# Performance work log

Hardware: AMD Instinct MI355X
Metric: run time of the kernel (lower is better)

## Reference

```python
import jax, jax.numpy as jnp
import numpy as np

P, D_IN, RANK, D_OUT, N = 64, 1024, 64, 1024, 4096


def setup_inputs() -> dict:
    key = jax.random.key(0)
    k1, k2, k3, k4, k5 = jax.random.split(key, 5)
    x = jax.random.normal(k1, (N, D_IN), dtype=jnp.float32)
    pids = jax.random.randint(k2, (N,), 0, P, dtype=jnp.int64)
    U = jax.random.normal(k3, (P, D_IN, RANK), dtype=jnp.float32) * 0.02
    V = jax.random.normal(k4, (P, RANK, D_OUT), dtype=jnp.float32) * 0.02
    bias = jax.random.normal(k5, (D_OUT,), dtype=jnp.float32)
    return {"x": x, "pids": pids, "U": U, "V": V, "bias": bias}


def reference(x, pids, U, V, bias):
    # Equivalent to: for each token n, out[n] = x[n] @ U[pids[n]] @ V[pids[n]] + bias
    # Computed as dense grouped GEMM over all partitions, then row-select by pid
    # (identical math to the masked per-partition loop in the torch module).
    h = jnp.einsum('nd,pdr->pnr', x, U)        # [P, N, R]
    o = jnp.einsum('pnr,pro->pno', h, V)       # [P, N, D_out]
    out = o[pids, jnp.arange(x.shape[0])] + bias  # select each token's own partition
    return out
```

## Files before the change

kernel.cpp:

```cpp
#include <hip/hip_runtime.h>
#include <hip/hip_bf16.h>

#define NP     64
#define D_IN   1024
#define RANK   64
#define D_OUT  1024
#define NTOK   4096
#define TM     64
#define BK     64
#define MT     128
#define KS     8
#define KW     (D_IN / KS)
#define OW     128
#define LDSTR  72

typedef __bf16 bf16x8 __attribute__((ext_vector_type(8)));
typedef float  f32x4  __attribute__((ext_vector_type(4)));

__device__ __forceinline__ unsigned short f2bf(float f) {
    unsigned u = __builtin_bit_cast(unsigned, f);
    u += 0x7FFFu + ((u >> 16) & 1u);
    return (unsigned short)(u >> 16);
}
__device__ __forceinline__ float bf2f(unsigned short s) {
    unsigned u = (unsigned)s << 16;
    return __builtin_bit_cast(float, u);
}
__device__ __forceinline__ bf16x8 pack8(float4 a, float4 b) {
    union { bf16x8 v; unsigned short s[8]; } r;
    r.s[0] = f2bf(a.x); r.s[1] = f2bf(a.y); r.s[2] = f2bf(a.z); r.s[3] = f2bf(a.w);
    r.s[4] = f2bf(b.x); r.s[5] = f2bf(b.y); r.s[6] = f2bf(b.z); r.s[7] = f2bf(b.w);
    return r.v;
}

__device__ __forceinline__ int swz_idx(int outer, int inner) {
    int blk = (inner >> 3) ^ ((outer >> 3) & 7);
    return outer * LDSTR + blk * 8 + (inner & 7);
}

__device__ __forceinline__ void decode_xcd(int b, int& tile, int& slice) {
    int g = b & 7;
    int l = b >> 3;
    slice = l >> 4;
    int m = l & 15;
    tile = (((m >> 1) << 3) | g) * 2 + (m & 1);
}

__global__ void bucket_kernel(const int* __restrict__ pids, int* __restrict__ meta) {
    __shared__ int counts[NP];
    __shared__ int cursor[NP];
    int tid = threadIdx.x;
    if (tid < NP) counts[tid] = 0;
    __syncthreads();
    for (int i = tid; i < NTOK / 4; i += 256) {
        int4 pv = reinterpret_cast<const int4*>(pids)[i];
        atomicAdd(&counts[pv.x & (NP - 1)], 1);
        atomicAdd(&counts[pv.y & (NP - 1)], 1);
        atomicAdd(&counts[pv.z & (NP - 1)], 1);
        atomicAdd(&counts[pv.w & (NP - 1)], 1);
    }
    __syncthreads();
    if (tid < 64) {
        int c = counts[tid];
        int ntp = (c + TM - 1) >> 6;
        int sc = c, st = ntp;
        for (int d = 1; d < 64; d <<= 1) {
            int vc = __shfl_up(sc, d);
            int vt = __shfl_up(st, d);
            if (tid >= d) { sc += vc; st += vt; }
        }
        int cbase = sc - c;
        int tb    = st - ntp;
        cursor[tid] = cbase;
        for (int t = 0; t < ntp; ++t) {
            int idx = tb + t;
            int rem = c - t * TM;
            int4 rec = {tid, cbase + t * TM, rem < TM ? rem : TM, 0};
            *reinterpret_cast<int4*>(meta + 16 + 4 * idx) = rec;
        }
        if (tid == 63) meta[0] = st;
    }
    __syncthreads();
    int* bucket = meta + 1024;
    for (int i = tid; i < NTOK / 4; i += 256) {
        int4 pv = reinterpret_cast<const int4*>(pids)[i];
        bucket[atomicAdd(&cursor[pv.x & (NP - 1)], 1)] = i * 4 + 0;
        bucket[atomicAdd(&cursor[pv.y & (NP - 1)], 1)] = i * 4 + 1;
        bucket[atomicAdd(&cursor[pv.z & (NP - 1)], 1)] = i * 4 + 2;
        bucket[atomicAdd(&cursor[pv.w & (NP - 1)], 1)] = i * 4 + 3;
    }
}

__global__ __launch_bounds__(256, 4) void h_kernel(
    const float* __restrict__ x, const float* __restrict__ U,
    const int* __restrict__ meta, unsigned short* __restrict__ Hpart)
{
    __shared__ __align__(16) unsigned short Us[2][RANK * LDSTR];
    __shared__ int toks[TM];

    int tile, ks;
    decode_xcd(blockIdx.x, tile, ks);
    int nt = meta[0];
    if (tile >= nt) return;
    int4 ti = *reinterpret_cast<const int4*>(meta + 16 + 4 * tile);
    int p = ti.x, off = ti.y, len = ti.z;

    int tid  = threadIdx.x;
    int lane = tid & 63;
    int w    = tid >> 6;
    int l15  = lane & 15;
    int l4   = lane >> 4;

    const int* bucket = meta + 1024;
    if (tid < TM) toks[tid] = (tid < len) ? bucket[off + tid] : -1;
    __syncthreads();

    int myrow = w * 16 + l15;
    int t = toks[myrow];
    bool valid = (t >= 0);
    const float* xrow = x + (size_t)(valid ? t : 0) * D_IN;
    const float* Up = U + (size_t)p * D_IN * RANK;

    int kbeg = ks * KW;
    int kk = tid >> 2;
    int q  = (tid & 3) * 16;

    float4 z{0,0,0,0};
    float4 c0a=z,c0b=z,c0c=z,c0d=z,c1a=z,c1b=z,c1c=z,c1d=z;
    if (valid) {
        const float* xp = xrow + kbeg + l4 * 8;
        c0a = *reinterpret_cast<const float4*>(xp);
        c0b = *reinterpret_cast<const float4*>(xp + 4);
        c0c = *reinterpret_cast<const float4*>(xp + 32);
        c0d = *reinterpret_cast<const float4*>(xp + 36);
        c1a = *reinterpret_cast<const float4*>(xp + 64);
        c1b = *reinterpret_cast<const float4*>(xp + 68);
        c1c = *reinterpret_cast<const float4*>(xp + 96);
        c1d = *reinterpret_cast<const float4*>(xp + 100);
    }

    f32x4 acc[4] = {};

    {
        const float* up = Up + (size_t)(kbeg + kk) * RANK + q;
#pragma unroll
        for (int i = 0; i < 4; ++i) {
            float4 v = *reinterpret_cast<const float4*>(up + i * 4);
            int r = q + i * 4;
            Us[0][swz_idx(r + 0, kk)] = f2bf(v.x);
            Us[0][swz_idx(r + 1, kk)] = f2bf(v.y);
            Us[0][swz_idx(r + 2, kk)] = f2bf(v.z);
            Us[0][swz_idx(r + 3, kk)] = f2bf(v.w);
        }
    }
    __syncthreads();

    float4 u10, u11, u12, u13;
    {
        const float* up = Up + (size_t)(kbeg + BK + kk) * RANK + q;
        u10 = *reinterpret_cast<const float4*>(up);
        u11 = *reinterpret_cast<const float4*>(up + 4);
        u12 = *reinterpret_cast<const float4*>(up + 8);
        u13 = *reinterpret_cast<const float4*>(up + 12);
    }

    {
        bf16x8 a0 = pack8(c0a, c0b);
        bf16x8 a1 = pack8(c0c, c0d);
#pragma unroll
        for (int k2 = 0; k2 < 2; ++k2) {
            int kof = k2 * 32 + l4 * 8;
            bf16x8 a = k2 ? a1 : a0;
#pragma unroll
            for (int ni = 0; ni < 4; ++ni) {
                bf16x8 b = *reinterpret_cast<const bf16x8*>(&Us[0][swz_idx(ni * 16 + l15, kof)]);
                acc[ni] = __builtin_amdgcn_mfma_f32_16x16x32_bf16(a, b, acc[ni], 0, 0, 0);
            }
        }
    }

    {
        float4 vv[4] = {u10, u11, u12, u13};
#pragma unroll
        for (int i = 0; i < 4; ++i) {
            int r = q + i * 4;
            Us[1][swz_idx(r + 0, kk)] = f2bf(vv[i].x);
            Us[1][swz_idx(r + 1, kk)] = f2bf(vv[i].y);
            Us[1][swz_idx(r + 2, kk)] = f2bf(vv[i].z);
            Us[1][swz_idx(r + 3, kk)] = f2bf(vv[i].w);
        }
    }
    __syncthreads();

    {
        bf16x8 a0 = pack8(c1a, c1b);
        bf16x8 a1 = pack8(c1c, c1d);
#pragma unroll
        for (int k2 = 0; k2 < 2; ++k2) {
            int kof = k2 * 32 + l4 * 8;
            bf16x8 a = k2 ? a1 : a0;
#pragma unroll
            for (int ni = 0; ni < 4; ++ni) {
                bf16x8 b = *reinterpret_cast<const bf16x8*>(&Us[1][swz_idx(ni * 16 + l15, kof)]);
                acc[ni] = __builtin_amdgcn_mfma_f32_16x16x32_bf16(a, b, acc[ni], 0, 0, 0);
            }
        }
    }

    unsigned short* hp = Hpart + ((size_t)ks * MT + tile) * (TM * RANK);
#pragma unroll
    for (int ni = 0; ni < 4; ++ni)
#pragma unroll
        for (int j = 0; j < 4; ++j) {
            int row = w * 16 + l4 * 4 + j;
            int col = ni * 16 + l15;
            hp[row * RANK + col] = f2bf(acc[ni][j]);
        }
}

__global__ __launch_bounds__(256, 4) void o_kernel(
    const float* __restrict__ V, const float* __restrict__ bias,
    const int* __restrict__ meta, const unsigned short* __restrict__ Hpart,
    float* __restrict__ out)
{
    __shared__ __align__(16) unsigned short Vs[OW * LDSTR];
    __shared__ int toks[TM];

    int tile, ocs;
    decode_xcd(blockIdx.x, tile, ocs);
    int oc = ocs * OW;
    int nt = meta[0];
    if (tile >= nt) return;
    int4 ti = *reinterpret_cast<const int4*>(meta + 16 + 4 * tile);
    int p = ti.x, off = ti.y, len = ti.z;

    int tid  = threadIdx.x;
    int lane = tid & 63;
    int w    = tid >> 6;
    int l15  = lane & 15;
    int l4   = lane >> 4;

    const int* bucket = meta + 1024;
    if (tid < TM) toks[tid] = (tid < len) ? bucket[off + tid] : -1;

    const float* Vp = V + (size_t)p * RANK * D_OUT;
    int o4 = (tid & 31) * 4;
    int rb = tid >> 5;
    float4 vv[8];
#pragma unroll
    for (int pass = 0; pass < 8; ++pass) {
        int r = pass * 8 + rb;
        vv[pass] = *reinterpret_cast<const float4*>(&Vp[(size_t)r * D_OUT + oc + o4]);
    }

    size_t hoff = (size_t)tile * (TM * RANK) + (w * 16 + l15) * RANK + l4 * 8;
    float s0[8] = {}, s1[8] = {};
#pragma unroll
    for (int k = 0; k < KS; ++k) {
        const unsigned short* pp = Hpart + (size_t)k * (MT * TM * RANK) + hoff;
        union { int4 i4; unsigned short u[8]; } va, vb;
        va.i4 = *reinterpret_cast<const int4*>(pp);
        vb.i4 = *reinterpret_cast<const int4*>(pp + 32);
#pragma unroll
        for (int j = 0; j < 8; ++j) { s0[j] += bf2f(va.u[j]); s1[j] += bf2f(vb.u[j]); }
    }
    union { bf16x8 v; unsigned short u[8]; } fa0, fa1;
#pragma unroll
    for (int j = 0; j < 8; ++j) { fa0.u[j] = f2bf(s0[j]); fa1.u[j] = f2bf(s1[j]); }

#pragma unroll
    for (int pass = 0; pass < 8; ++pass) {
        int r = pass * 8 + rb;
        Vs[swz_idx(o4 + 0, r)] = f2bf(vv[pass].x);
        Vs[swz_idx(o4 + 1, r)] = f2bf(vv[pass].y);
        Vs[swz_idx(o4 + 2, r)] = f2bf(vv[pass].z);
        Vs[swz_idx(o4 + 3, r)] = f2bf(vv[pass].w);
    }
    __syncthreads();

    f32x4 acc[8] = {};
#pragma unroll
    for (int k2 = 0; k2 < 2; ++k2) {
        int kof = k2 * 32 + l4 * 8;
        bf16x8 a = k2 ? fa1.v : fa0.v;
#pragma unroll
        for (int ni = 0; ni < 8; ++ni) {
            bf16x8 b = *reinterpret_cast<const bf16x8*>(&Vs[swz_idx(ni * 16 + l15, kof)]);
            acc[ni] = __builtin_amdgcn_mfma_f32_16x16x32_bf16(a, b, acc[ni], 0, 0, 0);
        }
    }

    int r0 = w * 16 + l4 * 4;
    int t0 = toks[r0 + 0], t1 = toks[r0 + 1], t2 = toks[r0 + 2], t3 = toks[r0 + 3];
#pragma unroll
    for (int ni = 0; ni < 8; ++ni) {
        int col = oc + ni * 16 + l15;
        float bv = bias[col];
        if (r0 + 0 < len) out[(size_t)t0 * D_OUT + col] = acc[ni][0] + bv;
        if (r0 + 1 < len) out[(size_t)t1 * D_OUT + col] = acc[ni][1] + bv;
        if (r0 + 2 < len) out[(size_t)t2 * D_OUT + col] = acc[ni][2] + bv;
        if (r0 + 3 < len) out[(size_t)t3 * D_OUT + col] = acc[ni][3] + bv;
    }
}

extern "C" void kernel_launch(void* const* d_in, const int* in_sizes, int n_in,
                              void* d_out, int out_size, void* d_ws, size_t ws_size,
                              hipStream_t stream) {
    const float* x    = (const float*)d_in[0];
    const int*   pids = (const int*)d_in[1];
    const float* U    = (const float*)d_in[2];
    const float* V    = (const float*)d_in[3];
    const float* bias = (const float*)d_in[4];
    float* out = (float*)d_out;

    int* meta = (int*)d_ws;
    unsigned short* Hpart = (unsigned short*)((char*)d_ws + 65536);

    bucket_kernel<<<1, 256, 0, stream>>>(pids, meta);
    h_kernel<<<MT * KS, 256, 0, stream>>>(x, U, meta, Hpart);
    o_kernel<<<MT * 8, 256, 0, stream>>>(V, bias, meta, Hpart, out);
}
```

Baseline: 37.74 us.

## Double K-split of h_kernel to one stage per block; read token ids directly

Result: slower. 45.75 us (+21.2%).

```diff
diff --git a/kernel.cpp b/kernel.cpp
--- a/kernel.cpp
+++ b/kernel.cpp
@@ -7,9 +7,8 @@
 #define D_OUT  1024
 #define NTOK   4096
 #define TM     64
-#define BK     64
 #define MT     128
-#define KS     8
+#define KS     16
 #define KW     (D_IN / KS)
 #define OW     128
 #define LDSTR  72
@@ -91,12 +90,11 @@
     }
 }
 
-__global__ __launch_bounds__(256, 4) void h_kernel(
+__global__ __launch_bounds__(256, 8) void h_kernel(
     const float* __restrict__ x, const float* __restrict__ U,
     const int* __restrict__ meta, unsigned short* __restrict__ Hpart)
 {
-    __shared__ __align__(16) unsigned short Us[2][RANK * LDSTR];
-    __shared__ int toks[TM];
+    __shared__ __align__(16) unsigned short Us[RANK * LDSTR];
 
     int tile, ks;
     decode_xcd(blockIdx.x, tile, ks);
@@ -111,97 +109,52 @@
     int l15  = lane & 15;
     int l4   = lane >> 4;
 
+    int myrow = w * 16 + l15;
     const int* bucket = meta + 1024;
-    if (tid < TM) toks[tid] = (tid < len) ? bucket[off + tid] : -1;
-    __syncthreads();
-
-    int myrow = w * 16 + l15;
-    int t = toks[myrow];
+    int t = (myrow < len) ? bucket[off + myrow] : -1;
     bool valid = (t >= 0);
     const float* xrow = x + (size_t)(valid ? t : 0) * D_IN;
     const float* Up = U + (size_t)p * D_IN * RANK;
 
     int kbeg = ks * KW;
-    int kk = tid >> 2;
-    int q  = (tid & 3) * 16;
 
     float4 z{0,0,0,0};
-    float4 c0a=z,c0b=z,c0c=z,c0d=z,c1a=z,c1b=z,c1c=z,c1d=z;
+    float4 xa=z, xb=z, xc=z, xd=z;
     if (valid) {
         const float* xp = xrow + kbeg + l4 * 8;
-        c0a = *reinterpret_cast<const float4*>(xp);
-        c0b = *reinterpret_cast<const float4*>(xp + 4);
-        c0c = *reinterpret_cast<const float4*>(xp + 32);
-        c0d = *reinterpret_cast<const float4*>(xp + 36);
-        c1a = *reinterpret_cast<const float4*>(xp + 64);
-        c1b = *reinterpret_cast<const float4*>(xp + 68);
-        c1c = *reinterpret_cast<const float4*>(xp + 96);
-        c1d = *reinterpret_cast<const float4*>(xp + 100);
-    }
-
-    f32x4 acc[4] = {};
+        xa = *reinterpret_cast<const float4*>(xp);
+        xb = *reinterpret_cast<const float4*>(xp + 4);
+        xc = *reinterpret_cast<const float4*>(xp + 32);
+        xd = *reinterpret_cast<const float4*>(xp + 36);
+    }
 
     {
+        int kk = tid >> 2;
+        int q  = (tid & 3) * 16;
         const float* up = Up + (size_t)(kbeg + kk) * RANK + q;
 #pragma unroll
         for (int i = 0; i < 4; ++i) {
             float4 v = *reinterpret_cast<const float4*>(up + i * 4);
             int r = q + i * 4;
-            Us[0][swz_idx(r + 0, kk)] = f2bf(v.x);
-            Us[0][swz_idx(r + 1, kk)] = f2bf(v.y);
-            Us[0][swz_idx(r + 2, kk)] = f2bf(v.z);
-            Us[0][swz_idx(r + 3, kk)] = f2bf(v.w);
-        }
-    }
-    __syncthreads();
-
-    float4 u10, u11, u12, u13;
+            Us[swz_idx(r + 0, kk)] = f2bf(v.x);
+            Us[swz_idx(r + 1, kk)] = f2bf(v.y);
+            Us[swz_idx(r + 2, kk)] = f2bf(v.z);
+            Us[swz_idx(r + 3, kk)] = f2bf(v.w);
+        }
+    }
+    __syncthreads();
+
+    f32x4 acc[4] = {};
     {
-        const float* up = Up + (size_t)(kbeg + BK + kk) * RANK + q;
-        u10 = *reinterpret_cast<const float4*>(up);
-        u11 = *reinterpret_cast<const float4*>(up + 4);
-        u12 = *reinterpret_cast<const float4*>(up + 8);
-        u13 = *reinterpret_cast<const float4*>(up + 12);
-    }
-
-    {
-        bf16x8 a0 = pack8(c0a, c0b);
-        bf16x8 a1 = pack8(c0c, c0d);
+        bf16x8 a0 = pack8(xa, xb);
+        bf16x8 a1 = pack8(xc, xd);
 #pragma unroll
         for (int k2 = 0; k2 < 2; ++k2) {
             int kof = k2 * 32 + l4 * 8;
             bf16x8 a = k2 ? a1 : a0;
 #pragma unroll
             for (int ni = 0; ni < 4; ++ni) {
-                bf16x8 b = *reinterpret_cast<const bf16x8*>(&Us[0][swz_idx(ni * 16 + l15, kof)]);
-                acc[ni] = __builtin_amdgcn_mfma_f32_16x16x32_bf16(a, b, acc[ni], 0, 0, 0);
-            }
-        }
-    }
-
-    {
-        float4 vv[4] = {u10, u11, u12, u13};
-#pragma unroll
-        for (int i = 0; i < 4; ++i) {
-            int r = q + i * 4;
-            Us[1][swz_idx(r + 0, kk)] = f2bf(vv[i].x);
-            Us[1][swz_idx(r + 1, kk)] = f2bf(vv[i].y);
-            Us[1][swz_idx(r + 2, kk)] = f2bf(vv[i].z);
-            Us[1][swz_idx(r + 3, kk)] = f2bf(vv[i].w);
-        }
-    }
-    __syncthreads();
-
-    {
-        bf16x8 a0 = pack8(c1a, c1b);
-        bf16x8 a1 = pack8(c1c, c1d);
-#pragma unroll
-        for (int k2 = 0; k2 < 2; ++k2) {
-            int kof = k2 * 32 + l4 * 8;
-            bf16x8 a = k2 ? a1 : a0;
-#pragma unroll
-            for (int ni = 0; ni < 4; ++ni) {
-                bf16x8 b = *reinterpret_cast<const bf16x8*>(&Us[1][swz_idx(ni * 16 + l15, kof)]);
+                bf16x8 b = *reinterpret_cast<const bf16x8*>(&Us[swz_idx(ni * 16 + l15, kof)]);
                 acc[ni] = __builtin_amdgcn_mfma_f32_16x16x32_bf16(a, b, acc[ni], 0, 0, 0);
             }
         }
@@ -224,7 +177,6 @@
     float* __restrict__ out)
 {
     __shared__ __align__(16) unsigned short Vs[OW * LDSTR];
-    __shared__ int toks[TM];
 
     int tile, ocs;
     decode_xcd(blockIdx.x, tile, ocs);
@@ -240,9 +192,6 @@
     int l15  = lane & 15;
     int l4   = lane >> 4;
 
-    const int* bucket = meta + 1024;
-    if (tid < TM) toks[tid] = (tid < len) ? bucket[off + tid] : -1;
-
     const float* Vp = V + (size_t)p * RANK * D_OUT;
     int o4 = (tid & 31) * 4;
     int rb = tid >> 5;
@@ -290,8 +239,10 @@
         }
     }
 
+    const int* bucket = meta + 1024;
     int r0 = w * 16 + l4 * 4;
-    int t0 = toks[r0 + 0], t1 = toks[r0 + 1], t2 = toks[r0 + 2], t3 = toks[r0 + 3];
+    int t0 = bucket[off + r0 + 0], t1 = bucket[off + r0 + 1];
+    int t2 = bucket[off + r0 + 2], t3 = bucket[off + r0 + 3];
 #pragma unroll
     for (int ni = 0; ni < 8; ++ni) {
         int col = oc + ni * 16 + l15;
```
